# Kernel tuning notes

Hardware: AMD Instinct MI355X
Metric: run time of the kernel (lower is better)

## Reference

```python
import jax, jax.numpy as jnp
import numpy as np

C = 2.0 + 1e-6
_nodes, _weights = np.polynomial.laguerre.laggauss(2)
QUAD_NODES = jnp.asarray(np.maximum(_nodes, 0.01) / C, dtype=jnp.float32)
QUAD_WEIGHTS = jnp.asarray(np.maximum(_weights, 0.01) / C, dtype=jnp.float32)
H, HD, P, M = 4, 64, 16, 32  # heads, head_dim, poly_dim, num_features
NUM_LABELS = 131072


def safe_normalize(x, axis=-1, eps=1e-4):
    n = jnp.linalg.norm(x, axis=axis, keepdims=True)
    return x / jnp.maximum(n, eps)


def safe_log(x, eps=1e-8):
    return jnp.log(jnp.maximum(x, eps))


def slay_features(x, omega, anchors):
    # x: [N, H*HD]; omega: [R,H,HD,M] (pre-scaled); anchors: [P,HD] (unit-norm)
    N = x.shape[0]
    xr = safe_normalize(x.reshape(N, H, HD), axis=-1)
    poly_proj = jnp.clip(jnp.einsum('nhd,pd->nhp', xr, anchors), -1.0, 1.0)
    poly_feat = poly_proj ** 2 / np.float32(np.sqrt(P))          # [N,H,P]
    prf_proj = jnp.einsum('nhd,rhdm->rnhm', xr, omega)           # [R,N,H,M]
    s = jnp.maximum(QUAD_NODES, 1e-6).reshape(-1, 1, 1, 1)
    exp_arg = jnp.clip(prf_proj * jnp.sqrt(2.0 * s) - s, -20.0, 20.0)
    prf_feat = jnp.exp(exp_arg) / np.float32(np.sqrt(M + 1e-6))
    prf_feat = prf_feat * jnp.sqrt(jnp.maximum(QUAD_WEIGHTS, 1e-6)).reshape(-1, 1, 1, 1)
    # fuse poly x prf, concat over quadrature nodes r (r-major feature order)
    fused = poly_feat[None, :, :, :, None] * prf_feat[:, :, :, None, :]  # [R,N,H,P,M]
    return fused.transpose(1, 0, 2, 3, 4).reshape(N, -1)         # [N, R*H*P*M]


def setup_inputs() -> dict:
    key = jax.random.key(0)
    ks = jax.random.split(key, 9)
    B, L, K = 1024, 128, 8
    return {
        'indices': jax.random.randint(ks[0], (B, L), 0, 100000),
        'mask': jnp.ones((B, L), dtype=jnp.float32),
        'labels': jax.random.randint(ks[1], (B, K), 0, NUM_LABELS),
        'label_mask': jnp.ones((B, K), dtype=jnp.float32),
        'neg_indices': jax.random.randint(ks[2], (2048,), 0, NUM_LABELS),
        'embed_table': jax.random.normal(ks[3], (100000, 256), dtype=jnp.float32),
        'kernel': jax.random.normal(ks[4], (256, NUM_LABELS), dtype=jnp.float32),
        'omega': jax.random.normal(ks[5], (2, H, HD, M), dtype=jnp.float32),
        'anchors': jax.random.normal(ks[6], (P, HD), dtype=jnp.float32),
    }


def reference(indices, mask, labels, label_mask, neg_indices, embed_table, kernel, omega, anchors):
    B, K = labels.shape
    # init-time parameter normalizations from the module
    omega_n = omega / np.float32(np.sqrt(HD))
    anchors_n = anchors / jnp.linalg.norm(anchors, axis=-1, keepdims=True)
    # MeanEmbedding encoder
    embeds = embed_table[indices]                                 # [B,L,D]
    summed = jnp.sum(embeds * mask[:, :, None], axis=1)
    query = summed / jnp.maximum(jnp.sum(mask, axis=1, keepdims=True), 1.0)
    query = safe_normalize(query, axis=-1)
    phi_query = slay_features(query, omega_n, anchors_n)          # [B,F]
    # sampled classifier rows
    W = safe_normalize(kernel.T, axis=-1)                         # [num_labels,D]
    safe_labels = jnp.maximum(labels, 0)
    all_needed = jnp.concatenate([safe_labels.reshape(-1), neg_indices])  # [B*K+Nneg]
    W_subset = W[all_needed]
    phi_W = slay_features(W_subset, omega_n, anchors_n)           # [B*K+Nneg,F]
    scores = phi_query @ phi_W.T                                  # [B, B*K+Nneg]
    idx_offsets = jnp.arange(B)[:, None] * K + jnp.arange(K)[None, :]
    pos_scores = jnp.take_along_axis(scores, idx_offsets, axis=1) # [B,K]
    neg_scores = scores[:, B * K:]                                # [B,Nneg]
    all_scores = jnp.concatenate([pos_scores, neg_scores], axis=1) + 1e-8
    log_Z = jax.scipy.special.logsumexp(safe_log(all_scores), axis=1)
    log_probs = safe_log(pos_scores + 1e-8) - log_Z[:, None]
    return -jnp.sum(log_probs * label_mask) / (jnp.sum(label_mask) + 1e-6)
```

## Files before the change

kernel.cpp:

```cpp
#include <hip/hip_runtime.h>
#include <math.h>

#define B_Q 1024
#define L_SEQ 128
#define D_EMB 256
#define NLAB 131072
#define LBL_ROWS 8192
#define NEG_ROWS 2048
#define W_ROWS 10240
#define CROW 320
#define LST 82
#define RPB 8

__device__ __forceinline__ float wave_sum(float v) {
#pragma unroll
  for (int off = 32; off > 0; off >>= 1) v += __shfl_xor(v, off, 64);
  return v;
}

__device__ __forceinline__ void slay_tail(const float* __restrict__ sx, int t,
                                          const float* __restrict__ anchT,
                                          const float* __restrict__ omega,
                                          float* __restrict__ outrow) {
  if (t < 64) {
    const int h = t >> 4, p = t & 15;
    const float* x = sx + h * 64;
    float d = 0.f;
#pragma unroll
    for (int dd = 0; dd < 64; dd++) d = fmaf(x[dd], anchT[dd * 16 + p], d);
    d = fminf(fmaxf(d, -1.0f), 1.0f);
    outrow[h * 16 + p] = d * d * 0.25f;
  }
  {
    const int r = t >> 7;
    const int h = (t >> 5) & 3;
    const float* x = sx + h * 64;
    const float* om = omega + (size_t)(t >> 5) * 2048 + (t & 31);
    float d = 0.f;
#pragma unroll
    for (int dd = 0; dd < 64; dd++) d = fmaf(x[dd], om[dd * 32], d);
    const float proj = d * 0.125f;
    const float s = r ? 1.70710592763316f : 0.29289307236691f;
    const float w = r ? 0.07322326809171f : 0.42677648190829f;
    float arg = proj * sqrtf(2.0f * s) - s;
    arg = fminf(fmaxf(arg, -20.0f), 20.0f);
    outrow[64 + t] = expf(arg) * (sqrtf(w) / sqrtf(32.000001f));
  }
}

__global__ __launch_bounds__(256) void k_setup(const float* __restrict__ anchors,
                                               const int* __restrict__ labels,
                                               const int* __restrict__ negidx,
                                               float* __restrict__ anchT,
                                               float* __restrict__ negparts,
                                               int* __restrict__ jidx,
                                               int* __restrict__ sorted) {
  __shared__ int shist[2048];
  __shared__ int s2[256];
  const int t = threadIdx.x, bx = blockIdx.x;
  if (bx == 0) {
    if (t < 64) {
      for (int p = 0; p < 16; p++) {
        const float v = anchors[p * 64 + t];
        const float n = sqrtf(wave_sum(v * v));
        anchT[t * 16 + p] = v / n;
      }
    }
  } else if (bx <= 256) {
    negparts[(bx - 1) * 256 + t] = 0.f;
  } else {
    for (int i = t; i < 2048; i += 256) shist[i] = 0;
    __syncthreads();
    for (int i = t; i < W_ROWS; i += 256) {
      int j;
      if (i < LBL_ROWS) { j = labels[i]; if (j < 0) j = 0; }
      else               { j = negidx[i - LBL_ROWS]; }
      jidx[i] = j;
      atomicAdd(&shist[j >> 6], 1);
    }
    __syncthreads();
    int v[8]; int sum = 0;
#pragma unroll
    for (int e = 0; e < 8; e++) { v[e] = shist[t * 8 + e]; sum += v[e]; }
    s2[t] = sum; __syncthreads();
    for (int off = 1; off < 256; off <<= 1) {
      const int x = s2[t];
      const int y = (t >= off) ? s2[t - off] : 0;
      __syncthreads();
      s2[t] = x + y;
      __syncthreads();
    }
    int run = s2[t] - sum;
#pragma unroll
    for (int e = 0; e < 8; e++) { shist[t * 8 + e] = run; run += v[e]; }
    __syncthreads();
    for (int i = t; i < W_ROWS; i += 256) {
      const int p = atomicAdd(&shist[jidx[i] >> 6], 1);
      sorted[p] = i;
    }
  }
}

__global__ __launch_bounds__(256) void k_feat(const int* __restrict__ indices,
                                              const float* __restrict__ mask,
                                              const float* __restrict__ embed,
                                              const float* __restrict__ kern,
                                              const float* __restrict__ anchT,
                                              const float* __restrict__ omega,
                                              const int* __restrict__ jidx,
                                              const int* __restrict__ sorted,
                                              float* __restrict__ qcomp,
                                              float* __restrict__ wcomp) {
  __shared__ __align__(16) float smem[2112];
  const int tid = threadIdx.x;

  if (blockIdx.x < B_Q) {
    const int b = blockIdx.x, t = tid;
    const int wv = t >> 6, ln = t & 63;
    int* sidx = (int*)smem;
    float* smask = smem + 128;
    float4* spart = (float4*)(smem + 256);
    float* smsum = smem + 1280;
    float* sx = smem + 1296;
    if (t < L_SEQ) { sidx[t] = indices[b * L_SEQ + t]; smask[t] = mask[b * L_SEQ + t]; }
    __syncthreads();
    float4 acc = {0.f, 0.f, 0.f, 0.f};
    float msum = 0.f;
#pragma unroll 8
    for (int l = wv * 32; l < wv * 32 + 32; l++) {
      const float m = smask[l];
      msum += m;
      const float4 e = *(const float4*)(embed + (size_t)sidx[l] * D_EMB + ln * 4);
      acc.x = fmaf(e.x, m, acc.x); acc.y = fmaf(e.y, m, acc.y);
      acc.z = fmaf(e.z, m, acc.z); acc.w = fmaf(e.w, m, acc.w);
    }
    spart[wv * 64 + ln] = acc;
    if (ln == 0) smsum[wv] = msum;
    __syncthreads();
    const float* spf = (const float*)spart;
    float q = spf[t] + spf[256 + t] + spf[512 + t] + spf[768 + t];
    const float mt = smsum[0] + smsum[1] + smsum[2] + smsum[3];
    q /= fmaxf(mt, 1.0f);
    const float ss = wave_sum(q * q);
    sx[t] = q / fmaxf(sqrtf(ss), 1e-4f);
    __syncthreads();
    slay_tail(sx, t, anchT, omega, qcomp + (size_t)b * CROW);
  } else {
    const int lb = blockIdx.x - B_Q;
    int* sj = (int*)smem;
    int* ssid = (int*)smem + 8;
    float* snorm = smem + 16;
    float* sx = smem + 48;
    const int cb = (lb & 7) * 160 + (lb >> 3);
    const int i0 = cb * RPB;

    if (tid < RPB) {
      const int sid = sorted[i0 + tid];
      ssid[tid] = sid;
      sj[tid] = jidx[sid];
    }
    __syncthreads();

#pragma unroll
    for (int k = 0; k < RPB; k++) {
      const int idx = k * 256 + tid;
      sx[idx] = kern[(size_t)(idx & 255) * NLAB + sj[idx >> 8]];
    }
    __syncthreads();

    {
      const int row = tid >> 5, sub = tid & 31;
      const float* xp = sx + row * 256 + sub * 8;
      float ssum = 0.f;
#pragma unroll
      for (int e = 0; e < 8; e++) ssum = fmaf(xp[e], xp[e], ssum);
      ssum += __shfl_xor(ssum, 1, 64);
      ssum += __shfl_xor(ssum, 2, 64);
      ssum += __shfl_xor(ssum, 4, 64);
      if ((sub & 7) == 0) snorm[row * 4 + (sub >> 3)] = fmaxf(sqrtf(ssum), 1e-4f);
    }
    __syncthreads();
#pragma unroll
    for (int k = 0; k < RPB; k++) {
      const int idx = k * 256 + tid;
      sx[idx] /= snorm[(idx >> 8) * 4 + ((idx >> 6) & 3)];
    }
    __syncthreads();

    {
      const int h = (tid >> 5) & 3, r = tid >> 7;
      const float* om = omega + (size_t)(tid >> 5) * 2048 + (tid & 31);
      float acc[RPB];
#pragma unroll
      for (int row = 0; row < RPB; row++) acc[row] = 0.f;
#pragma unroll
      for (int dd = 0; dd < 64; dd += 2) {
        const float o0 = om[dd * 32], o1 = om[dd * 32 + 32];
#pragma unroll
        for (int row = 0; row < RPB; row++) {
          const float2 xv = *(const float2*)(sx + row * 256 + h * 64 + dd);
          acc[row] = fmaf(xv.x, o0, fmaf(xv.y, o1, acc[row]));
        }
      }
      const float s = r ? 1.70710592763316f : 0.29289307236691f;
      const float w = r ? 0.07322326809171f : 0.42677648190829f;
      const float sc = sqrtf(2.0f * s);
      const float outs = sqrtf(w) / sqrtf(32.000001f);
#pragma unroll
      for (int row = 0; row < RPB; row++) {
        float arg = acc[row] * 0.125f * sc - s;
        arg = fminf(fmaxf(arg, -20.0f), 20.0f);
        wcomp[(size_t)ssid[row] * CROW + 64 + tid] = expf(arg) * outs;
      }
    }

    {
      const int hp = tid & 63, rp = tid >> 6;
      const int h = hp >> 4, p = hp & 15;
      const float* x0 = sx + (rp * 2) * 256 + h * 64;
      const float* x1 = x0 + 256;
      float d0 = 0.f, d1 = 0.f;
#pragma unroll
      for (int dd = 0; dd < 64; dd++) {
        const float a = anchT[dd * 16 + p];
        d0 = fmaf(x0[dd], a, d0);
        d1 = fmaf(x1[dd], a, d1);
      }
      d0 = fminf(fmaxf(d0, -1.0f), 1.0f);
      d1 = fminf(fmaxf(d1, -1.0f), 1.0f);
      wcomp[(size_t)ssid[rp * 2] * CROW + h * 16 + p]     = d0 * d0 * 0.25f;
      wcomp[(size_t)ssid[rp * 2 + 1] * CROW + h * 16 + p] = d1 * d1 * 0.25f;
    }
  }
}

__global__ __launch_bounds__(128) void k_score(const float* __restrict__ qcomp,
                                               const float* __restrict__ wcomp,
                                               float* __restrict__ negparts,
                                               float* __restrict__ pos) {
  __shared__ float qt[64 * LST];
  __shared__ float wt[32 * LST];
  const int tid = threadIdx.x;

  if (blockIdx.x < 4096) {
    const int qb0 = (blockIdx.x & 15) * 64;
    const int wb  = (blockIdx.x >> 4) & 63;
    const int wr0 = LBL_ROWS + wb * 32;
    const int h   = blockIdx.x >> 10;

    for (int idx = tid; idx < 96 * 20; idx += 128) {
      const int row = idx / 20, c4 = idx % 20;
      int col, lcol;
      if (c4 < 4)       { col = h * 16 + c4 * 4;              lcol = c4 * 4; }
      else if (c4 < 12) { col = 64 + h * 32 + (c4 - 4) * 4;   lcol = 16 + (c4 - 4) * 4; }
      else              { col = 192 + h * 32 + (c4 - 12) * 4; lcol = 48 + (c4 - 12) * 4; }
      const bool isq = row < 64;
      const int grow = isq ? (qb0 + row) : (wr0 + row - 64);
      const float4 v = *(const float4*)((isq ? qcomp : wcomp) + (size_t)grow * CROW + col);
      float* dst = (isq ? qt + row * LST : wt + (row - 64) * LST) + lcol;
      dst[0] = v.x; dst[1] = v.y; dst[2] = v.z; dst[3] = v.w;
    }
    __syncthreads();

    const int qg = tid >> 3;
    const int wg = tid & 7;
    const float* qb = qt + (qg * 4) * LST;
    const float* wbp = wt + (wg * 4) * LST;

    float pd[4][4] = {{0.f}}, pf[4][4] = {{0.f}};
#pragma unroll
    for (int kc = 0; kc < 8; kc++) {
      float2 qv[4], wv[4];
#pragma unroll
      for (int i = 0; i < 4; i++) qv[i] = *(const float2*)(qb + i * LST + 2 * kc);
#pragma unroll
      for (int j = 0; j < 4; j++) wv[j] = *(const float2*)(wbp + j * LST + 2 * kc);
#pragma unroll
      for (int i = 0; i < 4; i++)
#pragma unroll
        for (int j = 0; j < 4; j++) {
          pd[i][j] = fmaf(qv[i].x, wv[j].x, pd[i][j]);
          pd[i][j] = fmaf(qv[i].y, wv[j].y, pd[i][j]);
        }
    }
#pragma unroll 8
    for (int kc = 0; kc < 32; kc++) {
      float2 qv[4], wv[4];
#pragma unroll
      for (int i = 0; i < 4; i++) qv[i] = *(const float2*)(qb + i * LST + 16 + 2 * kc);
#pragma unroll
      for (int j = 0; j < 4; j++) wv[j] = *(const float2*)(wbp + j * LST + 16 + 2 * kc);
#pragma unroll
      for (int i = 0; i < 4; i++)
#pragma unroll
        for (int j = 0; j < 4; j++) {
          pf[i][j] = fmaf(qv[i].x, wv[j].x, pf[i][j]);
          pf[i][j] = fmaf(qv[i].y, wv[j].y, pf[i][j]);
        }
    }

#pragma unroll
    for (int i = 0; i < 4; i++) {
      float acc = 0.f;
#pragma unroll
      for (int j = 0; j < 4; j++) acc += pd[i][j] * pf[i][j];
#pragma unroll
      for (int off = 1; off < 8; off <<= 1) acc += __shfl_xor(acc, off, 64);
      if (wg == 0) atomicAdd(&negparts[wb * B_Q + qb0 + qg * 4 + i], acc);
    }
  } else {
    const int g = (blockIdx.x - 4096) * 32 + (tid >> 2);
    const int h = tid & 3;
    const float* q = qcomp + (size_t)(g >> 3) * CROW;
    const float* w = wcomp + (size_t)g * CROW;
    float pd = 0.f, pf = 0.f;
#pragma unroll
    for (int c = 0; c < 4; c++) {
      const float4 qv = *(const float4*)(q + h * 16 + c * 4);
      const float4 wv = *(const float4*)(w + h * 16 + c * 4);
      pd += qv.x * wv.x + qv.y * wv.y + qv.z * wv.z + qv.w * wv.w;
    }
#pragma unroll
    for (int r = 0; r < 2; r++)
#pragma unroll
      for (int c = 0; c < 8; c++) {
        const float4 qv = *(const float4*)(q + 64 + r * 128 + h * 32 + c * 4);
        const float4 wv = *(const float4*)(w + 64 + r * 128 + h * 32 + c * 4);
        pf += qv.x * wv.x + qv.y * wv.y + qv.z * wv.z + qv.w * wv.w;
      }
    float sc = pd * pf;
    sc += __shfl_xor(sc, 1, 64);
    sc += __shfl_xor(sc, 2, 64);
    if (h == 0) pos[g] = sc;
  }
}

__global__ __launch_bounds__(1024) void k_loss(const float* __restrict__ pos,
                                               const float* __restrict__ negparts,
                                               const float* __restrict__ lmask,
                                               float* __restrict__ out) {
  const int b = threadIdx.x;
  float lp[8];
  float possum = 0.f;
#pragma unroll
  for (int k = 0; k < 8; k++) { lp[k] = pos[b * 8 + k]; possum += lp[k]; }
  float negsum = 0.f;
#pragma unroll 8
  for (int c = 0; c < 64; c++) negsum += negparts[c * B_Q + b];
  const float Z = possum + negsum + 2.056e-5f;
  const float logZ = logf(Z);
  float local = 0.f, lsum = 0.f;
#pragma unroll
  for (int k = 0; k < 8; k++) {
    const float lm = lmask[b * 8 + k];
    local += lm * (logf(lp[k] + 1e-8f) - logZ);
    lsum += lm;
  }
  local = wave_sum(local);
  lsum = wave_sum(lsum);
  __shared__ float r1[16], r2[16];
  const int wid = b >> 6;
  if ((b & 63) == 0) { r1[wid] = local; r2[wid] = lsum; }
  __syncthreads();
  if (b == 0) {
    float t1 = 0.f, t2 = 0.f;
    for (int wv = 0; wv < 16; wv++) { t1 += r1[wv]; t2 += r2[wv]; }
    out[0] = -t1 / (t2 + 1e-6f);
  }
}

extern "C" void kernel_launch(void* const* d_in, const int* in_sizes, int n_in,
                              void* d_out, int out_size, void* d_ws, size_t ws_size,
                              hipStream_t stream) {
  const int* indices  = (const int*)d_in[0];
  const float* mask   = (const float*)d_in[1];
  const int* labels   = (const int*)d_in[2];
  const float* lmask  = (const float*)d_in[3];
  const int* negidx   = (const int*)d_in[4];
  const float* embed  = (const float*)d_in[5];
  const float* kern   = (const float*)d_in[6];
  const float* omega  = (const float*)d_in[7];
  const float* anchors= (const float*)d_in[8];
  float* out = (float*)d_out;

  float* ws = (float*)d_ws;
  float* anchT    = ws;
  float* qcomp    = anchT + 1024;
  float* wcomp    = qcomp + (size_t)B_Q * CROW;
  float* pos      = wcomp + (size_t)W_ROWS * CROW;
  float* negparts = pos + LBL_ROWS;
  int*   jidx     = (int*)(negparts + 64 * B_Q);
  int*   sorted   = jidx + W_ROWS;

  k_setup<<<258, 256, 0, stream>>>(anchors, labels, negidx, anchT, negparts, jidx, sorted);
  k_feat<<<B_Q + W_ROWS / RPB, 256, 0, stream>>>(indices, mask, embed, kern, anchT, omega,
                                                 jidx, sorted, qcomp, wcomp);
  k_score<<<4096 + 256, 128, 0, stream>>>(qcomp, wcomp, negparts, pos);
  k_loss<<<1, 1024, 0, stream>>>(pos, negparts, lmask, out);
}
```

Before: 370.1 us.

## Process 32 sorted label rows per block with coalesced gathers and folded norms

The classifier-row feature path now handles 32 sorted label rows per block instead of 8. The gather is reorganised so each warp's lanes read 32 nearby label columns of the same kernel row, which improves coalescing because the rows are bucket-sorted by label. Per-head normalisation is folded into the projections as a reciprocal-norm multiply, removing a separate divide pass over shared memory, and the shared tile is padded to avoid bank conflicts. The histogram/sort setup also moves to vectorised int4 loads. In exchange, shared memory grows, the block count drops by 4x and register pressure rises under the new launch bounds.

Result: faster. 355.2 us (-4.0%).

```diff
diff --git a/kernel.cpp b/kernel.cpp
--- a/kernel.cpp
+++ b/kernel.cpp
@@ -10,7 +10,8 @@
 #define W_ROWS 10240
 #define CROW 320
 #define LST 82
-#define RPB 8
+#define RPB 32
+#define SXS 258
 
 __device__ __forceinline__ float wave_sum(float v) {
 #pragma unroll
@@ -71,12 +72,23 @@
   } else {
     for (int i = t; i < 2048; i += 256) shist[i] = 0;
     __syncthreads();
-    for (int i = t; i < W_ROWS; i += 256) {
-      int j;
-      if (i < LBL_ROWS) { j = labels[i]; if (j < 0) j = 0; }
-      else               { j = negidx[i - LBL_ROWS]; }
-      jidx[i] = j;
-      atomicAdd(&shist[j >> 6], 1);
+    int4 lv[8], nv[2];
+#pragma unroll
+    for (int e = 0; e < 8; e++) {
+      int4 v = ((const int4*)labels)[e * 256 + t];
+      v.x = max(v.x, 0); v.y = max(v.y, 0); v.z = max(v.z, 0); v.w = max(v.w, 0);
+      lv[e] = v;
+      ((int4*)jidx)[e * 256 + t] = v;
+      atomicAdd(&shist[v.x >> 6], 1); atomicAdd(&shist[v.y >> 6], 1);
+      atomicAdd(&shist[v.z >> 6], 1); atomicAdd(&shist[v.w >> 6], 1);
+    }
+#pragma unroll
+    for (int e = 0; e < 2; e++) {
+      const int4 v = ((const int4*)negidx)[e * 256 + t];
+      nv[e] = v;
+      ((int4*)jidx)[2048 + e * 256 + t] = v;
+      atomicAdd(&shist[v.x >> 6], 1); atomicAdd(&shist[v.y >> 6], 1);
+      atomicAdd(&shist[v.z >> 6], 1); atomicAdd(&shist[v.w >> 6], 1);
     }
     __syncthreads();
     int v[8]; int sum = 0;
@@ -94,24 +106,36 @@
 #pragma unroll
     for (int e = 0; e < 8; e++) { shist[t * 8 + e] = run; run += v[e]; }
     __syncthreads();
-    for (int i = t; i < W_ROWS; i += 256) {
-      const int p = atomicAdd(&shist[jidx[i] >> 6], 1);
-      sorted[p] = i;
-    }
-  }
-}
-
-__global__ __launch_bounds__(256) void k_feat(const int* __restrict__ indices,
-                                              const float* __restrict__ mask,
-                                              const float* __restrict__ embed,
-                                              const float* __restrict__ kern,
-                                              const float* __restrict__ anchT,
-                                              const float* __restrict__ omega,
-                                              const int* __restrict__ jidx,
-                                              const int* __restrict__ sorted,
-                                              float* __restrict__ qcomp,
-                                              float* __restrict__ wcomp) {
-  __shared__ __align__(16) float smem[2112];
+#pragma unroll
+    for (int e = 0; e < 8; e++) {
+      const int i = (e * 256 + t) * 4;
+      sorted[atomicAdd(&shist[lv[e].x >> 6], 1)] = i;
+      sorted[atomicAdd(&shist[lv[e].y >> 6], 1)] = i + 1;
+      sorted[atomicAdd(&shist[lv[e].z >> 6], 1)] = i + 2;
+      sorted[atomicAdd(&shist[lv[e].w >> 6], 1)] = i + 3;
+    }
+#pragma unroll
+    for (int e = 0; e < 2; e++) {
+      const int i = LBL_ROWS + (e * 256 + t) * 4;
+      sorted[atomicAdd(&shist[nv[e].x >> 6], 1)] = i;
+      sorted[atomicAdd(&shist[nv[e].y >> 6], 1)] = i + 1;
+      sorted[atomicAdd(&shist[nv[e].z >> 6], 1)] = i + 2;
+      sorted[atomicAdd(&shist[nv[e].w >> 6], 1)] = i + 3;
+    }
+  }
+}
+
+__global__ __launch_bounds__(256, 4) void k_feat(const int* __restrict__ indices,
+                                                 const float* __restrict__ mask,
+                                                 const float* __restrict__ embed,
+                                                 const float* __restrict__ kern,
+                                                 const float* __restrict__ anchT,
+                                                 const float* __restrict__ omega,
+                                                 const int* __restrict__ jidx,
+                                                 const int* __restrict__ sorted,
+                                                 float* __restrict__ qcomp,
+                                                 float* __restrict__ wcomp) {
+  __shared__ __align__(16) float smem[9504];
   const int tid = threadIdx.x;
 
   if (blockIdx.x < B_Q) {
@@ -148,10 +172,11 @@
   } else {
     const int lb = blockIdx.x - B_Q;
     int* sj = (int*)smem;
-    int* ssid = (int*)smem + 8;
-    float* snorm = smem + 16;
-    float* sx = smem + 48;
-    const int cb = (lb & 7) * 160 + (lb >> 3);
+    int* ssid = (int*)smem + 32;
+    float* rnorm = smem + 64;
+    float* sq = smem + 192;
+    float* sx = smem + 1248;
+    const int cb = (lb & 7) * 40 + (lb >> 3);
     const int i0 = cb * RPB;
 
     if (tid < RPB) {
@@ -161,75 +186,82 @@
     }
     __syncthreads();
 
-#pragma unroll
-    for (int k = 0; k < RPB; k++) {
-      const int idx = k * 256 + tid;
-      sx[idx] = kern[(size_t)(idx & 255) * NLAB + sj[idx >> 8]];
-    }
-    __syncthreads();
-
     {
-      const int row = tid >> 5, sub = tid & 31;
-      const float* xp = sx + row * 256 + sub * 8;
-      float ssum = 0.f;
-#pragma unroll
-      for (int e = 0; e < 8; e++) ssum = fmaf(xp[e], xp[e], ssum);
-      ssum += __shfl_xor(ssum, 1, 64);
-      ssum += __shfl_xor(ssum, 2, 64);
-      ssum += __shfl_xor(ssum, 4, 64);
-      if ((sub & 7) == 0) snorm[row * 4 + (sub >> 3)] = fmaxf(sqrtf(ssum), 1e-4f);
-    }
-    __syncthreads();
-#pragma unroll
-    for (int k = 0; k < RPB; k++) {
-      const int idx = k * 256 + tid;
-      sx[idx] /= snorm[(idx >> 8) * 4 + ((idx >> 6) & 3)];
+      const int row = tid & 31, dloc = tid >> 5;
+      const float* kbase = kern + ((size_t)dloc << 17) + (size_t)sj[row];
+      float ssq[4] = {0.f, 0.f, 0.f, 0.f};
+#pragma unroll
+      for (int it = 0; it < 32; it++) {
+        const float v = kbase[(size_t)it << 20];
+        sx[row * SXS + it * 8 + dloc] = v;
+        ssq[it >> 3] = fmaf(v, v, ssq[it >> 3]);
+      }
+#pragma unroll
+      for (int h = 0; h < 4; h++) sq[row * 33 + dloc * 4 + h] = ssq[h];
+    }
+    __syncthreads();
+    if (tid < 128) {
+      const int r2 = tid >> 2, h = tid & 3;
+      float s = 0.f;
+#pragma unroll
+      for (int dl = 0; dl < 8; dl++) s += sq[r2 * 33 + dl * 4 + h];
+      rnorm[r2 * 4 + h] = 1.0f / fmaxf(sqrtf(s), 1e-4f);
     }
     __syncthreads();
 
     {
-      const int h = (tid >> 5) & 3, r = tid >> 7;
+      const int hh = (tid >> 5) & 3, r = tid >> 7;
       const float* om = omega + (size_t)(tid >> 5) * 2048 + (tid & 31);
-      float acc[RPB];
-#pragma unroll
-      for (int row = 0; row < RPB; row++) acc[row] = 0.f;
-#pragma unroll
-      for (int dd = 0; dd < 64; dd += 2) {
-        const float o0 = om[dd * 32], o1 = om[dd * 32 + 32];
-#pragma unroll
-        for (int row = 0; row < RPB; row++) {
-          const float2 xv = *(const float2*)(sx + row * 256 + h * 64 + dd);
-          acc[row] = fmaf(xv.x, o0, fmaf(xv.y, o1, acc[row]));
-        }
-      }
       const float s = r ? 1.70710592763316f : 0.29289307236691f;
       const float w = r ? 0.07322326809171f : 0.42677648190829f;
       const float sc = sqrtf(2.0f * s);
       const float outs = sqrtf(w) / sqrtf(32.000001f);
 #pragma unroll
-      for (int row = 0; row < RPB; row++) {
-        float arg = acc[row] * 0.125f * sc - s;
-        arg = fminf(fmaxf(arg, -20.0f), 20.0f);
-        wcomp[(size_t)ssid[row] * CROW + 64 + tid] = expf(arg) * outs;
+      for (int half = 0; half < 2; half++) {
+        float acc[16];
+#pragma unroll
+        for (int rq = 0; rq < 16; rq++) acc[rq] = 0.f;
+#pragma unroll
+        for (int dd = 0; dd < 64; dd += 2) {
+          const float o0 = om[dd * 32], o1 = om[dd * 32 + 32];
+#pragma unroll
+          for (int rq = 0; rq < 16; rq++) {
+            const float2 xv = *(const float2*)(sx + (half * 16 + rq) * SXS + hh * 64 + dd);
+            acc[rq] = fmaf(xv.x, o0, fmaf(xv.y, o1, acc[rq]));
+          }
+        }
+#pragma unroll
+        for (int rq = 0; rq < 16; rq++) {
+          const int row = half * 16 + rq;
+          float arg = acc[rq] * 0.125f * rnorm[row * 4 + hh] * sc - s;
+          arg = fminf(fmaxf(arg, -20.0f), 20.0f);
+          wcomp[(size_t)ssid[row] * CROW + 64 + tid] = expf(arg) * outs;
+        }
       }
     }
 
     {
       const int hp = tid & 63, rp = tid >> 6;
       const int h = hp >> 4, p = hp & 15;
-      const float* x0 = sx + (rp * 2) * 256 + h * 64;
-      const float* x1 = x0 + 256;
-      float d0 = 0.f, d1 = 0.f;
-#pragma unroll
-      for (int dd = 0; dd < 64; dd++) {
-        const float a = anchT[dd * 16 + p];
-        d0 = fmaf(x0[dd], a, d0);
-        d1 = fmaf(x1[dd], a, d1);
+#pragma unroll
+      for (int pr = 0; pr < 4; pr++) {
+        const int r0 = rp * 8 + pr * 2;
+        const float* x0 = sx + r0 * SXS + h * 64;
+        const float* x1 = x0 + SXS;
+        float d0 = 0.f, d1 = 0.f;
+#pragma unroll
+        for (int dd = 0; dd < 64; dd++) {
+          const float a = anchT[dd * 16 + p];
+          d0 = fmaf(x0[dd], a, d0);
+          d1 = fmaf(x1[dd], a, d1);
+        }
+        d0 *= rnorm[r0 * 4 + h];
+        d1 *= rnorm[(r0 + 1) * 4 + h];
+        d0 = fminf(fmaxf(d0, -1.0f), 1.0f);
+        d1 = fminf(fmaxf(d1, -1.0f), 1.0f);
+        wcomp[(size_t)ssid[r0] * CROW + h * 16 + p]     = d0 * d0 * 0.25f;
+        wcomp[(size_t)ssid[r0 + 1] * CROW + h * 16 + p] = d1 * d1 * 0.25f;
       }
-      d0 = fminf(fmaxf(d0, -1.0f), 1.0f);
-      d1 = fminf(fmaxf(d1, -1.0f), 1.0f);
-      wcomp[(size_t)ssid[rp * 2] * CROW + h * 16 + p]     = d0 * d0 * 0.25f;
-      wcomp[(size_t)ssid[rp * 2 + 1] * CROW + h * 16 + p] = d1 * d1 * 0.25f;
     }
   }
 }
```
